# Kernel tuning notes

Measured on AMD Instinct MI355X. Metric: run time of the kernel, lower is better.

Reference implementation:

```python
import jax, jax.numpy as jnp
import numpy as np

N_NODES = 50000
N_EDGES = 800000
IN_C, HID_C, OUT_C, N_CLASSES = 256, 128, 128, 6
N_GRAPHS = 256
BN_EPS = 1e-5


def setup_inputs() -> dict:
    key = jax.random.key(0)
    ks = jax.random.split(key, 24)
    inp = {
        "x": jax.random.normal(ks[0], (N_NODES, IN_C), dtype=jnp.float32),
        "edge_index": jax.random.randint(ks[1], (2, N_EDGES), 0, N_NODES, dtype=jnp.int64),
        "batch": jnp.sort(jax.random.randint(ks[2], (N_NODES,), 0, N_GRAPHS, dtype=jnp.int64)),
    }
    dims = [(IN_C, HID_C), (HID_C, HID_C), (HID_C, OUT_C)]
    k = 3
    for i, (ci, co) in enumerate(dims):
        scale = 1.0 / np.sqrt(ci)
        inp[f"W{i}"] = jax.random.uniform(ks[k], (ci, co), minval=-scale, maxval=scale); k += 1
        inp[f"b{i}"] = jax.random.uniform(ks[k], (co,), minval=-scale, maxval=scale); k += 1
        inp[f"g{i}"] = jax.random.uniform(ks[k], (co,), minval=0.5, maxval=1.5); k += 1
        inp[f"bt{i}"] = 0.1 * jax.random.normal(ks[k], (co,)); k += 1
        inp[f"m{i}"] = 0.1 * jax.random.normal(ks[k], (co,)); k += 1
        inp[f"v{i}"] = jax.random.uniform(ks[k], (co,), minval=0.5, maxval=1.5); k += 1
    scale = 1.0 / np.sqrt(OUT_C)
    inp["lin_W"] = jax.random.uniform(ks[k], (OUT_C, N_CLASSES), minval=-scale, maxval=scale); k += 1
    inp["lin_b"] = jax.random.uniform(ks[k], (N_CLASSES,), minval=-scale, maxval=scale)
    return inp


def gcn_conv(x, W, b, row, col, n):
    # PyG GCNConv: linear transform, add self-loops, symmetric degree norm, scatter-add
    h = x @ W  # [N, Co]
    loop = jnp.arange(n, dtype=row.dtype)
    r = jnp.concatenate([row, loop])
    c = jnp.concatenate([col, loop])
    deg = jax.ops.segment_sum(jnp.ones_like(c, dtype=h.dtype), c, num_segments=n)
    dinv = jax.lax.rsqrt(deg)  # deg >= 1 thanks to self-loops
    norm = dinv[r] * dinv[c]  # [E+N]
    msg = h[r] * norm[:, None]
    return jax.ops.segment_sum(msg, c, num_segments=n) + b


def batch_norm(x, g, bt, m, v):
    return (x - m) * jax.lax.rsqrt(v + BN_EPS) * g + bt


def reference(x, edge_index, batch,
              W0, b0, g0, bt0, m0, v0,
              W1, b1, g1, bt1, m1, v1,
              W2, b2, g2, bt2, m2, v2,
              lin_W, lin_b):
    row, col = edge_index[0], edge_index[1]
    n = x.shape[0]
    params = [(W0, b0, g0, bt0, m0, v0), (W1, b1, g1, bt1, m1, v1), (W2, b2, g2, bt2, m2, v2)]
    h = x
    for (W, b, g, bt, m, v) in params:
        h = gcn_conv(h, W, b, row, col, n)
        h = batch_norm(h, g, bt, m, v)
        h = jax.nn.relu(h)  # dropout is identity in eval mode
    # global mean pool over graphs
    sums = jax.ops.segment_sum(h, batch, num_segments=N_GRAPHS)
    cnts = jax.ops.segment_sum(jnp.ones((n,), dtype=h.dtype), batch, num_segments=N_GRAPHS)
    pooled = sums / jnp.maximum(cnts, 1.0)[:, None]
    return pooled @ lin_W + lin_b  # [N_GRAPHS, N_CLASSES]
```

## Files before the change

kernel.cpp:

```cpp
#include <hip/hip_runtime.h>
#include <hip/hip_bf16.h>

#define N_NODES   50000
#define N_EDGES   800000
#define IN_C      256
#define HID_C     128
#define N_GRAPHS  256
#define N_CLASSES 6
#define BN_EPS    1e-5f

using bf16x8 = __attribute__((ext_vector_type(8))) short;
using f32x4  = __attribute__((ext_vector_type(4))) float;

__device__ __forceinline__ ushort f2bf(float f) {
    union { float f; unsigned u; } v; v.f = f;
    unsigned r = v.u + 0x7fffu + ((v.u >> 16) & 1u);
    return (ushort)(r >> 16);
}
__device__ __forceinline__ float bflo(unsigned u) {
    union { unsigned u; float f; } v; v.u = u << 16; return v.f;
}
__device__ __forceinline__ float bfhi(unsigned u) {
    union { unsigned u; float f; } v; v.u = u & 0xffff0000u; return v.f;
}

__global__ void k_init(int* ecnt, int n) {
    int i = blockIdx.x * blockDim.x + threadIdx.x;
    if (i < n) ecnt[i] = 0;
}

__global__ void k_count_rank(const int* __restrict__ col, int* __restrict__ ecnt,
                             int* __restrict__ rank, int e) {
    int i0 = (blockIdx.x * blockDim.x + threadIdx.x) * 4;
    if (i0 + 3 < e) {
        int4 c = *reinterpret_cast<const int4*>(col + i0);
        int4 r;
        r.x = atomicAdd(&ecnt[c.x], 1);
        r.y = atomicAdd(&ecnt[c.y], 1);
        r.z = atomicAdd(&ecnt[c.z], 1);
        r.w = atomicAdd(&ecnt[c.w], 1);
        *reinterpret_cast<int4*>(rank + i0) = r;
    } else {
        for (int i = i0; i < e; ++i) rank[i] = atomicAdd(&ecnt[col[i]], 1);
    }
}

__global__ void k_scanA(const int* __restrict__ ecnt, int* __restrict__ row_ptr,
                        int* __restrict__ bsum, float* __restrict__ dinv, int n) {
    __shared__ int s[256];
    int t = threadIdx.x;
    int i = blockIdx.x * 256 + t;
    int v = (i < n) ? ecnt[i] : 0;
    if (i < n) dinv[i] = rsqrtf((float)(v + 1));
    s[t] = v;
    __syncthreads();
    for (int d = 1; d < 256; d <<= 1) {
        int add = (t >= d) ? s[t - d] : 0;
        __syncthreads();
        s[t] += add;
        __syncthreads();
    }
    if (i < n) row_ptr[i] = s[t];
    if (t == 255) bsum[blockIdx.x] = s[255];
}

__global__ void k_scanB(const int* __restrict__ bsum, int* __restrict__ bsumx, int nb) {
    __shared__ int s[256];
    int t = threadIdx.x;
    int v = (t < nb) ? bsum[t] : 0;
    s[t] = v;
    __syncthreads();
    for (int d = 1; d < 256; d <<= 1) {
        int add = (t >= d) ? s[t - d] : 0;
        __syncthreads();
        s[t] += add;
        __syncthreads();
    }
    bsumx[t] = s[t] - v;
}

__global__ void k_scanC(const int* __restrict__ ecnt, int* __restrict__ row_ptr,
                        const int* __restrict__ bsumx, int n, int e) {
    int i = blockIdx.x * 256 + threadIdx.x;
    if (i < n) row_ptr[i] = row_ptr[i] - ecnt[i] + bsumx[blockIdx.x];
    if (i == 0) row_ptr[n] = e;
}

__global__ void k_fill(const int* __restrict__ row, const int* __restrict__ col,
                       const int* __restrict__ row_ptr, const int* __restrict__ rank,
                       const float* __restrict__ dinv, int2* __restrict__ wedge, int e) {
    int i0 = (blockIdx.x * blockDim.x + threadIdx.x) * 4;
    if (i0 + 3 < e) {
        int4 c  = *reinterpret_cast<const int4*>(col + i0);
        int4 r  = *reinterpret_cast<const int4*>(row + i0);
        int4 rk = *reinterpret_cast<const int4*>(rank + i0);
        wedge[row_ptr[c.x] + rk.x] = make_int2(r.x, __float_as_int(dinv[r.x]));
        wedge[row_ptr[c.y] + rk.y] = make_int2(r.y, __float_as_int(dinv[r.y]));
        wedge[row_ptr[c.z] + rk.z] = make_int2(r.z, __float_as_int(dinv[r.z]));
        wedge[row_ptr[c.w] + rk.w] = make_int2(r.w, __float_as_int(dinv[r.w]));
    } else {
        for (int i = i0; i < e; ++i)
            wedge[row_ptr[col[i]] + rank[i]] = make_int2(row[i], __float_as_int(dinv[row[i]]));
    }
}

__global__ void k_prepWF(const float* __restrict__ W0, const float* __restrict__ W1,
                         const float* __restrict__ W2, ushort* __restrict__ Wt0,
                         ushort* __restrict__ Wt1, ushort* __restrict__ Wt2,
                         const float* __restrict__ b0, const float* __restrict__ g0,
                         const float* __restrict__ bt0, const float* __restrict__ m0,
                         const float* __restrict__ v0,
                         const float* __restrict__ b1, const float* __restrict__ g1,
                         const float* __restrict__ bt1, const float* __restrict__ m1,
                         const float* __restrict__ v1,
                         const float* __restrict__ b2, const float* __restrict__ g2,
                         const float* __restrict__ bt2, const float* __restrict__ m2,
                         const float* __restrict__ v2,
                         float* __restrict__ fA, float* __restrict__ fC) {
    int t = blockIdx.x * blockDim.x + threadIdx.x;
    const int NW0 = 128 * IN_C, NW1 = 128 * HID_C;
    if (t < NW0) {
        int co = t / IN_C, k = t % IN_C;
        Wt0[t] = f2bf(W0[(size_t)k * 128 + co]);
    } else if (t < NW0 + NW1) {
        int u = t - NW0;
        int co = u / HID_C, k = u % HID_C;
        Wt1[u] = f2bf(W1[(size_t)k * 128 + co]);
    } else if (t < NW0 + 2 * NW1) {
        int u = t - NW0 - NW1;
        int co = u / HID_C, k = u % HID_C;
        Wt2[u] = f2bf(W2[(size_t)k * 128 + co]);
    } else if (t < NW0 + 2 * NW1 + 3 * 128) {
        int u = t - NW0 - 2 * NW1;
        int layer = u >> 7, c = u & 127;
        const float *b_, *g_, *bt_, *m_, *v_;
        if (layer == 0)      { b_ = b0; g_ = g0; bt_ = bt0; m_ = m0; v_ = v0; }
        else if (layer == 1) { b_ = b1; g_ = g1; bt_ = bt1; m_ = m1; v_ = v1; }
        else                 { b_ = b2; g_ = g2; bt_ = bt2; m_ = m2; v_ = v2; }
        float A = g_[c] * rsqrtf(v_[c] + BN_EPS);
        fA[u] = A;
        fC[u] = (b_[c] - m_[c]) * A + bt_[c];
    }
}

template <int K, bool AFP32>
__global__ __launch_bounds__(256) void k_gemmbf(const void* __restrict__ Av,
                                                const ushort* __restrict__ Wt,
                                                ushort* __restrict__ Cbf, int M) {
    extern __shared__ char smem[];
    const int tid = threadIdx.x;
    constexpr int CPC = K / 8;
    constexpr int NCH = 128 * CPC;
    for (int c = tid; c < NCH; c += 256) {
        int col = c / CPC, kg = c % CPC;
        float4 v = *reinterpret_cast<const float4*>(Wt + (size_t)col * K + kg * 8);
        int dst = col * (K * 2) + ((kg * 16) ^ ((col & 7) << 4));
        *reinterpret_cast<float4*>(smem + dst) = v;
    }
    __syncthreads();

    const int wave = tid >> 6, lane = tid & 63;
    const int l15 = lane & 15, lg = lane >> 4;
    const int row = blockIdx.x * 64 + wave * 16 + l15;
    const bool rok = (row < M);

    f32x4 acc[8] = {};

#pragma unroll
    for (int ks = 0; ks < K / 32; ++ks) {
        bf16x8 a;
        if (AFP32) {
            const float* Ap = (const float*)Av + (size_t)row * K + ks * 32 + lg * 8;
            float4 f0, f1;
            if (rok) {
                f0 = *reinterpret_cast<const float4*>(Ap);
                f1 = *reinterpret_cast<const float4*>(Ap + 4);
            } else {
                f0 = make_float4(0, 0, 0, 0); f1 = f0;
            }
            a[0] = (short)f2bf(f0.x); a[1] = (short)f2bf(f0.y);
            a[2] = (short)f2bf(f0.z); a[3] = (short)f2bf(f0.w);
            a[4] = (short)f2bf(f1.x); a[5] = (short)f2bf(f1.y);
            a[6] = (short)f2bf(f1.z); a[7] = (short)f2bf(f1.w);
        } else {
            if (rok) {
                const ushort* Ap = (const ushort*)Av + (size_t)row * K + ks * 32 + lg * 8;
                a = *reinterpret_cast<const bf16x8*>(Ap);
            } else {
#pragma unroll
                for (int j = 0; j < 8; ++j) a[j] = 0;
            }
        }
#pragma unroll
        for (int cf = 0; cf < 8; ++cf) {
            int col = cf * 16 + l15;
            int off = col * (K * 2) + ((ks * 64 + lg * 16) ^ ((col & 7) << 4));
            bf16x8 b = *reinterpret_cast<const bf16x8*>(smem + off);
            acc[cf] = __builtin_amdgcn_mfma_f32_16x16x32_bf16(a, b, acc[cf], 0, 0, 0);
        }
    }

#pragma unroll
    for (int cf = 0; cf < 8; ++cf) {
        int col = cf * 16 + l15;
#pragma unroll
        for (int i = 0; i < 4; ++i) {
            int r = blockIdx.x * 64 + wave * 16 + lg * 4 + i;
            if (r < M) Cbf[(size_t)r * 128 + col] = f2bf(acc[cf][i]);
        }
    }
}

__global__ __launch_bounds__(256) void k_aggbf(const ushort* __restrict__ h,
                                               const int* __restrict__ row_ptr,
                                               const int2* __restrict__ wedge,
                                               const float* __restrict__ dinv,
                                               const float* __restrict__ fA,
                                               const float* __restrict__ fC,
                                               ushort* __restrict__ out, int n) {
    int wave = threadIdx.x >> 6, lane = threadIdx.x & 63;
    int vtx = blockIdx.x * 4 + wave;
    if (vtx >= n) return;
    int q = lane >> 4, l15 = lane & 15;
    int c0 = l15 * 8;
    int beg = row_ptr[vtx], end = row_ptr[vtx + 1];

    float a0 = 0.f, a1 = 0.f, a2 = 0.f, a3 = 0.f;
    float a4 = 0.f, a5 = 0.f, a6 = 0.f, a7 = 0.f;
    for (int e = beg + q; e < end; e += 16) {
        int eB = e + 4, eC = e + 8, eD = e + 12;
        bool kB = eB < end, kC = eC < end, kD = eD < end;
        int2 wd0 = wedge[e];
        int2 wd1 = wedge[kB ? eB : e];
        int2 wd2 = wedge[kC ? eC : e];
        int2 wd3 = wedge[kD ? eD : e];
        float w0 = __int_as_float(wd0.y);
        float w1 = kB ? __int_as_float(wd1.y) : 0.f;
        float w2 = kC ? __int_as_float(wd2.y) : 0.f;
        float w3 = kD ? __int_as_float(wd3.y) : 0.f;
        uint4 u0 = *reinterpret_cast<const uint4*>(h + (size_t)wd0.x * 128 + c0);
        uint4 u1 = *reinterpret_cast<const uint4*>(h + (size_t)wd1.x * 128 + c0);
        uint4 u2 = *reinterpret_cast<const uint4*>(h + (size_t)wd2.x * 128 + c0);
        uint4 u3 = *reinterpret_cast<const uint4*>(h + (size_t)wd3.x * 128 + c0);
        a0 = fmaf(bflo(u0.x), w0, a0); a1 = fmaf(bfhi(u0.x), w0, a1);
        a2 = fmaf(bflo(u0.y), w0, a2); a3 = fmaf(bfhi(u0.y), w0, a3);
        a4 = fmaf(bflo(u0.z), w0, a4); a5 = fmaf(bfhi(u0.z), w0, a5);
        a6 = fmaf(bflo(u0.w), w0, a6); a7 = fmaf(bfhi(u0.w), w0, a7);
        a0 = fmaf(bflo(u1.x), w1, a0); a1 = fmaf(bfhi(u1.x), w1, a1);
        a2 = fmaf(bflo(u1.y), w1, a2); a3 = fmaf(bfhi(u1.y), w1, a3);
        a4 = fmaf(bflo(u1.z), w1, a4); a5 = fmaf(bfhi(u1.z), w1, a5);
        a6 = fmaf(bflo(u1.w), w1, a6); a7 = fmaf(bfhi(u1.w), w1, a7);
        a0 = fmaf(bflo(u2.x), w2, a0); a1 = fmaf(bfhi(u2.x), w2, a1);
        a2 = fmaf(bflo(u2.y), w2, a2); a3 = fmaf(bfhi(u2.y), w2, a3);
        a4 = fmaf(bflo(u2.z), w2, a4); a5 = fmaf(bfhi(u2.z), w2, a5);
        a6 = fmaf(bflo(u2.w), w2, a6); a7 = fmaf(bfhi(u2.w), w2, a7);
        a0 = fmaf(bflo(u3.x), w3, a0); a1 = fmaf(bfhi(u3.x), w3, a1);
        a2 = fmaf(bflo(u3.y), w3, a2); a3 = fmaf(bfhi(u3.y), w3, a3);
        a4 = fmaf(bflo(u3.z), w3, a4); a5 = fmaf(bfhi(u3.z), w3, a5);
        a6 = fmaf(bflo(u3.w), w3, a6); a7 = fmaf(bfhi(u3.w), w3, a7);
    }

    a0 += __shfl_xor(a0, 16); a0 += __shfl_xor(a0, 32);
    a1 += __shfl_xor(a1, 16); a1 += __shfl_xor(a1, 32);
    a2 += __shfl_xor(a2, 16); a2 += __shfl_xor(a2, 32);
    a3 += __shfl_xor(a3, 16); a3 += __shfl_xor(a3, 32);
    a4 += __shfl_xor(a4, 16); a4 += __shfl_xor(a4, 32);
    a5 += __shfl_xor(a5, 16); a5 += __shfl_xor(a5, 32);
    a6 += __shfl_xor(a6, 16); a6 += __shfl_xor(a6, 32);
    a7 += __shfl_xor(a7, 16); a7 += __shfl_xor(a7, 32);

    if (q == 0) {
        float dv = dinv[vtx];
        float dvv = dv * dv;
        uint4 us = *reinterpret_cast<const uint4*>(h + (size_t)vtx * 128 + c0);
        float4 A0 = *reinterpret_cast<const float4*>(fA + c0);
        float4 A1 = *reinterpret_cast<const float4*>(fA + c0 + 4);
        float4 C0 = *reinterpret_cast<const float4*>(fC + c0);
        float4 C1 = *reinterpret_cast<const float4*>(fC + c0 + 4);
        float v0 = fmaf(a0, dv * A0.x, fmaf(bflo(us.x), dvv * A0.x, C0.x));
        float v1 = fmaf(a1, dv * A0.y, fmaf(bfhi(us.x), dvv * A0.y, C0.y));
        float v2 = fmaf(a2, dv * A0.z, fmaf(bflo(us.y), dvv * A0.z, C0.z));
        float v3 = fmaf(a3, dv * A0.w, fmaf(bfhi(us.y), dvv * A0.w, C0.w));
        float v4 = fmaf(a4, dv * A1.x, fmaf(bflo(us.z), dvv * A1.x, C1.x));
        float v5 = fmaf(a5, dv * A1.y, fmaf(bfhi(us.z), dvv * A1.y, C1.y));
        float v6 = fmaf(a6, dv * A1.z, fmaf(bflo(us.w), dvv * A1.z, C1.z));
        float v7 = fmaf(a7, dv * A1.w, fmaf(bfhi(us.w), dvv * A1.w, C1.w));
        v0 = fmaxf(v0, 0.f); v1 = fmaxf(v1, 0.f); v2 = fmaxf(v2, 0.f); v3 = fmaxf(v3, 0.f);
        v4 = fmaxf(v4, 0.f); v5 = fmaxf(v5, 0.f); v6 = fmaxf(v6, 0.f); v7 = fmaxf(v7, 0.f);
        uint4 packed;
        packed.x = (unsigned)f2bf(v0) | ((unsigned)f2bf(v1) << 16);
        packed.y = (unsigned)f2bf(v2) | ((unsigned)f2bf(v3) << 16);
        packed.z = (unsigned)f2bf(v4) | ((unsigned)f2bf(v5) << 16);
        packed.w = (unsigned)f2bf(v6) | ((unsigned)f2bf(v7) << 16);
        *reinterpret_cast<uint4*>(out + (size_t)vtx * 128 + c0) = packed;
    }
}

__global__ __launch_bounds__(256) void k_poolfinal(const ushort* __restrict__ h,
                                                   const int* __restrict__ batch,
                                                   const float* __restrict__ lw,
                                                   const float* __restrict__ lb,
                                                   float* __restrict__ out, int n) {
    __shared__ float psum[4][128];
    __shared__ float pool[128];
    int g = blockIdx.x;
    int tid = threadIdx.x;
    int wave = tid >> 6, lane = tid & 63;
    int lo = 0, hi = n;
    while (lo < hi) { int m = (lo + hi) >> 1; if (batch[m] < g) lo = m + 1; else hi = m; }
    int a = lo;
    lo = 0; hi = n;
    int g1 = g + 1;
    while (lo < hi) { int m = (lo + hi) >> 1; if (batch[m] < g1) lo = m + 1; else hi = m; }
    int b = lo;

    int c0 = lane * 2;
    float a0 = 0.f, a1 = 0.f;
    int i = a + wave;
    for (; i + 12 < b; i += 16) {
        unsigned u0 = *reinterpret_cast<const unsigned*>(h + (size_t)i * 128 + c0);
        unsigned u1 = *reinterpret_cast<const unsigned*>(h + (size_t)(i + 4) * 128 + c0);
        unsigned u2 = *reinterpret_cast<const unsigned*>(h + (size_t)(i + 8) * 128 + c0);
        unsigned u3 = *reinterpret_cast<const unsigned*>(h + (size_t)(i + 12) * 128 + c0);
        a0 += bflo(u0) + bflo(u1) + bflo(u2) + bflo(u3);
        a1 += bfhi(u0) + bfhi(u1) + bfhi(u2) + bfhi(u3);
    }
    for (; i < b; i += 4) {
        unsigned u = *reinterpret_cast<const unsigned*>(h + (size_t)i * 128 + c0);
        a0 += bflo(u); a1 += bfhi(u);
    }
    psum[wave][c0] = a0;
    psum[wave][c0 + 1] = a1;
    __syncthreads();
    if (tid < 128) pool[tid] = psum[0][tid] + psum[1][tid] + psum[2][tid] + psum[3][tid];
    __syncthreads();
    if (tid < N_CLASSES) {
        float inv = 1.0f / fmaxf((float)(b - a), 1.0f);
        float s = 0.f;
        for (int k = 0; k < 128; ++k) s = fmaf(pool[k], lw[k * N_CLASSES + tid], s);
        out[g * N_CLASSES + tid] = s * inv + lb[tid];
    }
}

extern "C" void kernel_launch(void* const* d_in, const int* in_sizes, int n_in,
                              void* d_out, int out_size, void* d_ws, size_t ws_size,
                              hipStream_t stream) {
    const float* x      = (const float*)d_in[0];
    const int*   ei     = (const int*)d_in[1];
    const int*   batch  = (const int*)d_in[2];
    const float* W0  = (const float*)d_in[3];
    const float* b0  = (const float*)d_in[4];
    const float* g0  = (const float*)d_in[5];
    const float* bt0 = (const float*)d_in[6];
    const float* m0  = (const float*)d_in[7];
    const float* v0  = (const float*)d_in[8];
    const float* W1  = (const float*)d_in[9];
    const float* b1  = (const float*)d_in[10];
    const float* g1  = (const float*)d_in[11];
    const float* bt1 = (const float*)d_in[12];
    const float* m1  = (const float*)d_in[13];
    const float* v1  = (const float*)d_in[14];
    const float* W2  = (const float*)d_in[15];
    const float* b2  = (const float*)d_in[16];
    const float* g2  = (const float*)d_in[17];
    const float* bt2 = (const float*)d_in[18];
    const float* m2  = (const float*)d_in[19];
    const float* v2  = (const float*)d_in[20];
    const float* lw  = (const float*)d_in[21];
    const float* lb  = (const float*)d_in[22];
    float* out = (float*)d_out;

    const int N = in_sizes[2];
    const int E = in_sizes[1] / 2;
    const int* row = ei;
    const int* col = ei + E;

    char* ws = (char*)d_ws;
    size_t off = 0;
    auto alloc = [&](size_t bytes) {
        void* p = ws + off;
        off += (bytes + 511) & ~(size_t)511;
        return p;
    };
    ushort* hA     = (ushort*)alloc((size_t)N * 128 * 2);
    ushort* hB     = (ushort*)alloc((size_t)N * 128 * 2);
    ushort* Wt0    = (ushort*)alloc((size_t)128 * IN_C * 2);
    ushort* Wt1    = (ushort*)alloc((size_t)128 * HID_C * 2);
    ushort* Wt2    = (ushort*)alloc((size_t)128 * HID_C * 2);
    int*   ecnt    = (int*)alloc((size_t)N * 4);
    int*   rank    = (int*)alloc((size_t)E * 4);
    int*   row_ptr = (int*)alloc((size_t)(N + 1) * 4);
    int2*  wedge   = (int2*)alloc((size_t)E * 8);
    float* dinv    = (float*)alloc((size_t)N * 4);
    int*   bsum    = (int*)alloc(256 * 4);
    int*   bsumx   = (int*)alloc(256 * 4);
    float* fA      = (float*)alloc(3 * 128 * 4);
    float* fC      = (float*)alloc(3 * 128 * 4);

    const int NB_n  = (N + 255) / 256;
    const int NB_e4 = (E / 4 + 255) / 256;

    k_init<<<NB_n, 256, 0, stream>>>(ecnt, N);
    k_count_rank<<<NB_e4, 256, 0, stream>>>(col, ecnt, rank, E);
    k_scanA<<<NB_n, 256, 0, stream>>>(ecnt, row_ptr, bsum, dinv, N);
    k_scanB<<<1, 256, 0, stream>>>(bsum, bsumx, NB_n);
    k_scanC<<<NB_n, 256, 0, stream>>>(ecnt, row_ptr, bsumx, N, E);
    k_fill<<<NB_e4, 256, 0, stream>>>(row, col, row_ptr, rank, dinv, wedge, E);

    const int PW = (128 * (IN_C + 2 * HID_C) + 3 * 128 + 255) / 256;
    k_prepWF<<<PW, 256, 0, stream>>>(W0, W1, W2, Wt0, Wt1, Wt2,
                                     b0, g0, bt0, m0, v0,
                                     b1, g1, bt1, m1, v1,
                                     b2, g2, bt2, m2, v2, fA, fC);

    const int GB = (N + 63) / 64;
    const int AB = (N + 3) / 4;

    k_gemmbf<IN_C, true><<<GB, 256, IN_C * 128 * 2, stream>>>(x, Wt0, hB, N);
    k_aggbf<<<AB, 256, 0, stream>>>(hB, row_ptr, wedge, dinv, fA, fC, hA, N);
    k_gemmbf<HID_C, false><<<GB, 256, HID_C * 128 * 2, stream>>>(hA, Wt1, hB, N);
    k_aggbf<<<AB, 256, 0, stream>>>(hB, row_ptr, wedge, dinv, fA + 128, fC + 128, hA, N);
    k_gemmbf<HID_C, false><<<GB, 256, HID_C * 128 * 2, stream>>>(hA, Wt2, hB, N);
    k_aggbf<<<AB, 256, 0, stream>>>(hB, row_ptr, wedge, dinv, fA + 256, fC + 256, hA, N);

    k_poolfinal<<<N_GRAPHS, 256, 0, stream>>>(hA, batch, lw, lb, out, N);
}
```

Baseline: 228.1 us.

## Slice hidden features into 32-column planes for cache-local aggregation; merge setup kernels

Stores intermediate bf16 features as four column slices of 32 channels each, [4][N][32]. The aggregation kernel now processes one slice per block, with 16 lanes covering one vertex's 32 channels, so each gathered row is 64 bytes and a slice's working set is a quarter of the full feature matrix, which should improve L2 hit rates on the random neighbour gathers. The GEMM's A reads and C writes and the pooling reads are changed to match the sliced layout. Separately, the ecnt zeroing is folded into the weight-prep kernel and the two scan-fixup kernels are merged, removing two launches. In exchange, each vertex's edge list is now walked four times, once per slice, and the wedge indices are reloaded for each pass.

```diff
diff --git a/kernel.cpp b/kernel.cpp
--- a/kernel.cpp
+++ b/kernel.cpp
@@ -9,6 +9,7 @@
 #define N_CLASSES 6
 #define BN_EPS    1e-5f
 
+
 using bf16x8 = __attribute__((ext_vector_type(8))) short;
 using f32x4  = __attribute__((ext_vector_type(4))) float;
 
@@ -22,11 +23,6 @@
 }
 __device__ __forceinline__ float bfhi(unsigned u) {
     union { unsigned u; float f; } v; v.u = u & 0xffff0000u; return v.f;
-}
-
-__global__ void k_init(int* ecnt, int n) {
-    int i = blockIdx.x * blockDim.x + threadIdx.x;
-    if (i < n) ecnt[i] = 0;
 }
 
 __global__ void k_count_rank(const int* __restrict__ col, int* __restrict__ ecnt,
@@ -64,7 +60,8 @@
     if (t == 255) bsum[blockIdx.x] = s[255];
 }
 
-__global__ void k_scanB(const int* __restrict__ bsum, int* __restrict__ bsumx, int nb) {
+__global__ void k_scanC(const int* __restrict__ ecnt, int* __restrict__ row_ptr,
+                        const int* __restrict__ bsum, int nb, int n, int e) {
     __shared__ int s[256];
     int t = threadIdx.x;
     int v = (t < nb) ? bsum[t] : 0;
@@ -76,13 +73,9 @@
         s[t] += add;
         __syncthreads();
     }
-    bsumx[t] = s[t] - v;
-}
-
-__global__ void k_scanC(const int* __restrict__ ecnt, int* __restrict__ row_ptr,
-                        const int* __restrict__ bsumx, int n, int e) {
-    int i = blockIdx.x * 256 + threadIdx.x;
-    if (i < n) row_ptr[i] = row_ptr[i] - ecnt[i] + bsumx[blockIdx.x];
+    int off = (blockIdx.x > 0) ? s[blockIdx.x - 1] : 0;
+    int i = blockIdx.x * 256 + t;
+    if (i < n) row_ptr[i] = row_ptr[i] - ecnt[i] + off;
     if (i == 0) row_ptr[n] = e;
 }
 
@@ -116,8 +109,10 @@
                          const float* __restrict__ b2, const float* __restrict__ g2,
                          const float* __restrict__ bt2, const float* __restrict__ m2,
                          const float* __restrict__ v2,
-                         float* __restrict__ fA, float* __restrict__ fC) {
+                         float* __restrict__ fA, float* __restrict__ fC,
+                         int* __restrict__ ecnt, int n) {
     int t = blockIdx.x * blockDim.x + threadIdx.x;
+    if (t < n) ecnt[t] = 0;
     const int NW0 = 128 * IN_C, NW1 = 128 * HID_C;
     if (t < NW0) {
         int co = t / IN_C, k = t % IN_C;
@@ -184,7 +179,7 @@
             a[6] = (short)f2bf(f1.z); a[7] = (short)f2bf(f1.w);
         } else {
             if (rok) {
-                const ushort* Ap = (const ushort*)Av + (size_t)row * K + ks * 32 + lg * 8;
+                const ushort* Ap = (const ushort*)Av + (size_t)ks * M * 32 + (size_t)row * 32 + lg * 8;
                 a = *reinterpret_cast<const bf16x8*>(Ap);
             } else {
 #pragma unroll
@@ -202,11 +197,12 @@
 
 #pragma unroll
     for (int cf = 0; cf < 8; ++cf) {
-        int col = cf * 16 + l15;
+        int sl = cf >> 1;
+        int off = (cf & 1) * 16 + l15;
 #pragma unroll
         for (int i = 0; i < 4; ++i) {
             int r = blockIdx.x * 64 + wave * 16 + lg * 4 + i;
-            if (r < M) Cbf[(size_t)r * 128 + col] = f2bf(acc[cf][i]);
+            if (r < M) Cbf[(size_t)sl * M * 32 + (size_t)r * 32 + off] = f2bf(acc[cf][i]);
         }
     }
 }
@@ -218,82 +214,49 @@
                                                const float* __restrict__ fA,
                                                const float* __restrict__ fC,
                                                ushort* __restrict__ out, int n) {
-    int wave = threadIdx.x >> 6, lane = threadIdx.x & 63;
-    int vtx = blockIdx.x * 4 + wave;
+    const int slice = blockIdx.x & 3;
+    const int nb = blockIdx.x >> 2;
+    const int wave = threadIdx.x >> 6, lane = threadIdx.x & 63;
+    const int q = lane >> 4, l15 = lane & 15;
+    const int vtx = nb * 16 + wave * 4 + q;
     if (vtx >= n) return;
-    int q = lane >> 4, l15 = lane & 15;
-    int c0 = l15 * 8;
+    const ushort* hs = h + (size_t)slice * n * 32;
+    const int c0 = l15 * 2;
+
     int beg = row_ptr[vtx], end = row_ptr[vtx + 1];
-
-    float a0 = 0.f, a1 = 0.f, a2 = 0.f, a3 = 0.f;
-    float a4 = 0.f, a5 = 0.f, a6 = 0.f, a7 = 0.f;
-    for (int e = beg + q; e < end; e += 16) {
-        int eB = e + 4, eC = e + 8, eD = e + 12;
-        bool kB = eB < end, kC = eC < end, kD = eD < end;
+    float a0 = 0.f, a1 = 0.f;
+    for (int e = beg; e < end; e += 4) {
+        int e1 = e + 1, e2 = e + 2, e3 = e + 3;
+        bool k1 = e1 < end, k2 = e2 < end, k3 = e3 < end;
         int2 wd0 = wedge[e];
-        int2 wd1 = wedge[kB ? eB : e];
-        int2 wd2 = wedge[kC ? eC : e];
-        int2 wd3 = wedge[kD ? eD : e];
+        int2 wd1 = wedge[k1 ? e1 : e];
+        int2 wd2 = wedge[k2 ? e2 : e];
+        int2 wd3 = wedge[k3 ? e3 : e];
         float w0 = __int_as_float(wd0.y);
-        float w1 = kB ? __int_as_float(wd1.y) : 0.f;
-        float w2 = kC ? __int_as_float(wd2.y) : 0.f;
-        float w3 = kD ? __int_as_float(wd3.y) : 0.f;
-        uint4 u0 = *reinterpret_cast<const uint4*>(h + (size_t)wd0.x * 128 + c0);
-        uint4 u1 = *reinterpret_cast<const uint4*>(h + (size_t)wd1.x * 128 + c0);
-        uint4 u2 = *reinterpret_cast<const uint4*>(h + (size_t)wd2.x * 128 + c0);
-        uint4 u3 = *reinterpret_cast<const uint4*>(h + (size_t)wd3.x * 128 + c0);
-        a0 = fmaf(bflo(u0.x), w0, a0); a1 = fmaf(bfhi(u0.x), w0, a1);
-        a2 = fmaf(bflo(u0.y), w0, a2); a3 = fmaf(bfhi(u0.y), w0, a3);
-        a4 = fmaf(bflo(u0.z), w0, a4); a5 = fmaf(bfhi(u0.z), w0, a5);
-        a6 = fmaf(bflo(u0.w), w0, a6); a7 = fmaf(bfhi(u0.w), w0, a7);
-        a0 = fmaf(bflo(u1.x), w1, a0); a1 = fmaf(bfhi(u1.x), w1, a1);
-        a2 = fmaf(bflo(u1.y), w1, a2); a3 = fmaf(bfhi(u1.y), w1, a3);
-        a4 = fmaf(bflo(u1.z), w1, a4); a5 = fmaf(bfhi(u1.z), w1, a5);
-        a6 = fmaf(bflo(u1.w), w1, a6); a7 = fmaf(bfhi(u1.w), w1, a7);
-        a0 = fmaf(bflo(u2.x), w2, a0); a1 = fmaf(bfhi(u2.x), w2, a1);
-        a2 = fmaf(bflo(u2.y), w2, a2); a3 = fmaf(bfhi(u2.y), w2, a3);
-        a4 = fmaf(bflo(u2.z), w2, a4); a5 = fmaf(bfhi(u2.z), w2, a5);
-        a6 = fmaf(bflo(u2.w), w2, a6); a7 = fmaf(bfhi(u2.w), w2, a7);
-        a0 = fmaf(bflo(u3.x), w3, a0); a1 = fmaf(bfhi(u3.x), w3, a1);
-        a2 = fmaf(bflo(u3.y), w3, a2); a3 = fmaf(bfhi(u3.y), w3, a3);
-        a4 = fmaf(bflo(u3.z), w3, a4); a5 = fmaf(bfhi(u3.z), w3, a5);
-        a6 = fmaf(bflo(u3.w), w3, a6); a7 = fmaf(bfhi(u3.w), w3, a7);
-    }
-
-    a0 += __shfl_xor(a0, 16); a0 += __shfl_xor(a0, 32);
-    a1 += __shfl_xor(a1, 16); a1 += __shfl_xor(a1, 32);
-    a2 += __shfl_xor(a2, 16); a2 += __shfl_xor(a2, 32);
-    a3 += __shfl_xor(a3, 16); a3 += __shfl_xor(a3, 32);
-    a4 += __shfl_xor(a4, 16); a4 += __shfl_xor(a4, 32);
-    a5 += __shfl_xor(a5, 16); a5 += __shfl_xor(a5, 32);
-    a6 += __shfl_xor(a6, 16); a6 += __shfl_xor(a6, 32);
-    a7 += __shfl_xor(a7, 16); a7 += __shfl_xor(a7, 32);
-
-    if (q == 0) {
-        float dv = dinv[vtx];
-        float dvv = dv * dv;
-        uint4 us = *reinterpret_cast<const uint4*>(h + (size_t)vtx * 128 + c0);
-        float4 A0 = *reinterpret_cast<const float4*>(fA + c0);
-        float4 A1 = *reinterpret_cast<const float4*>(fA + c0 + 4);
-        float4 C0 = *reinterpret_cast<const float4*>(fC + c0);
-        float4 C1 = *reinterpret_cast<const float4*>(fC + c0 + 4);
-        float v0 = fmaf(a0, dv * A0.x, fmaf(bflo(us.x), dvv * A0.x, C0.x));
-        float v1 = fmaf(a1, dv * A0.y, fmaf(bfhi(us.x), dvv * A0.y, C0.y));
-        float v2 = fmaf(a2, dv * A0.z, fmaf(bflo(us.y), dvv * A0.z, C0.z));
-        float v3 = fmaf(a3, dv * A0.w, fmaf(bfhi(us.y), dvv * A0.w, C0.w));
-        float v4 = fmaf(a4, dv * A1.x, fmaf(bflo(us.z), dvv * A1.x, C1.x));
-        float v5 = fmaf(a5, dv * A1.y, fmaf(bfhi(us.z), dvv * A1.y, C1.y));
-        float v6 = fmaf(a6, dv * A1.z, fmaf(bflo(us.w), dvv * A1.z, C1.z));
-        float v7 = fmaf(a7, dv * A1.w, fmaf(bfhi(us.w), dvv * A1.w, C1.w));
-        v0 = fmaxf(v0, 0.f); v1 = fmaxf(v1, 0.f); v2 = fmaxf(v2, 0.f); v3 = fmaxf(v3, 0.f);
-        v4 = fmaxf(v4, 0.f); v5 = fmaxf(v5, 0.f); v6 = fmaxf(v6, 0.f); v7 = fmaxf(v7, 0.f);
-        uint4 packed;
-        packed.x = (unsigned)f2bf(v0) | ((unsigned)f2bf(v1) << 16);
-        packed.y = (unsigned)f2bf(v2) | ((unsigned)f2bf(v3) << 16);
-        packed.z = (unsigned)f2bf(v4) | ((unsigned)f2bf(v5) << 16);
-        packed.w = (unsigned)f2bf(v6) | ((unsigned)f2bf(v7) << 16);
-        *reinterpret_cast<uint4*>(out + (size_t)vtx * 128 + c0) = packed;
-    }
+        float w1 = k1 ? __int_as_float(wd1.y) : 0.f;
+        float w2 = k2 ? __int_as_float(wd2.y) : 0.f;
+        float w3 = k3 ? __int_as_float(wd3.y) : 0.f;
+        unsigned u0 = *reinterpret_cast<const unsigned*>(hs + (size_t)wd0.x * 32 + c0);
+        unsigned u1 = *reinterpret_cast<const unsigned*>(hs + (size_t)wd1.x * 32 + c0);
+        unsigned u2 = *reinterpret_cast<const unsigned*>(hs + (size_t)wd2.x * 32 + c0);
+        unsigned u3 = *reinterpret_cast<const unsigned*>(hs + (size_t)wd3.x * 32 + c0);
+        a0 = fmaf(bflo(u0), w0, a0); a1 = fmaf(bfhi(u0), w0, a1);
+        a0 = fmaf(bflo(u1), w1, a0); a1 = fmaf(bfhi(u1), w1, a1);
+        a0 = fmaf(bflo(u2), w2, a0); a1 = fmaf(bfhi(u2), w2, a1);
+        a0 = fmaf(bflo(u3), w3, a0); a1 = fmaf(bfhi(u3), w3, a1);
+    }
+
+    float dv = dinv[vtx];
+    float dvv = dv * dv;
+    unsigned us = *reinterpret_cast<const unsigned*>(hs + (size_t)vtx * 32 + c0);
+    int c = slice * 32 + c0;
+    float2 A = *reinterpret_cast<const float2*>(fA + c);
+    float2 C = *reinterpret_cast<const float2*>(fC + c);
+    float v0 = fmaf(a0, dv * A.x, fmaf(bflo(us), dvv * A.x, C.x));
+    float v1 = fmaf(a1, dv * A.y, fmaf(bfhi(us), dvv * A.y, C.y));
+    v0 = fmaxf(v0, 0.f); v1 = fmaxf(v1, 0.f);
+    unsigned packed = (unsigned)f2bf(v0) | ((unsigned)f2bf(v1) << 16);
+    *reinterpret_cast<unsigned*>(out + (size_t)slice * n * 32 + (size_t)vtx * 32 + c0) = packed;
 }
 
 __global__ __launch_bounds__(256) void k_poolfinal(const ushort* __restrict__ h,
@@ -314,21 +277,22 @@
     while (lo < hi) { int m = (lo + hi) >> 1; if (batch[m] < g1) lo = m + 1; else hi = m; }
     int b = lo;
 
-    int c0 = lane * 2;
+    const ushort* hs = h + (size_t)(lane >> 4) * n * 32 + (lane & 15) * 2;
     float a0 = 0.f, a1 = 0.f;
     int i = a + wave;
     for (; i + 12 < b; i += 16) {
-        unsigned u0 = *reinterpret_cast<const unsigned*>(h + (size_t)i * 128 + c0);
-        unsigned u1 = *reinterpret_cast<const unsigned*>(h + (size_t)(i + 4) * 128 + c0);
-        unsigned u2 = *reinterpret_cast<const unsigned*>(h + (size_t)(i + 8) * 128 + c0);
-        unsigned u3 = *reinterpret_cast<const unsigned*>(h + (size_t)(i + 12) * 128 + c0);
+        unsigned u0 = *reinterpret_cast<const unsigned*>(hs + (size_t)i * 32);
+        unsigned u1 = *reinterpret_cast<const unsigned*>(hs + (size_t)(i + 4) * 32);
+        unsigned u2 = *reinterpret_cast<const unsigned*>(hs + (size_t)(i + 8) * 32);
+        unsigned u3 = *reinterpret_cast<const unsigned*>(hs + (size_t)(i + 12) * 32);
         a0 += bflo(u0) + bflo(u1) + bflo(u2) + bflo(u3);
         a1 += bfhi(u0) + bfhi(u1) + bfhi(u2) + bfhi(u3);
     }
     for (; i < b; i += 4) {
-        unsigned u = *reinterpret_cast<const unsigned*>(h + (size_t)i * 128 + c0);
+        unsigned u = *reinterpret_cast<const unsigned*>(hs + (size_t)i * 32);
         a0 += bflo(u); a1 += bfhi(u);
     }
+    int c0 = lane * 2;
     psum[wave][c0] = a0;
     psum[wave][c0 + 1] = a1;
     __syncthreads();
@@ -393,28 +357,24 @@
     int2*  wedge   = (int2*)alloc((size_t)E * 8);
     float* dinv    = (float*)alloc((size_t)N * 4);
     int*   bsum    = (int*)alloc(256 * 4);
-    int*   bsumx   = (int*)alloc(256 * 4);
     float* fA      = (float*)alloc(3 * 128 * 4);
     float* fC      = (float*)alloc(3 * 128 * 4);
 
     const int NB_n  = (N + 255) / 256;
     const int NB_e4 = (E / 4 + 255) / 256;
-
-    k_init<<<NB_n, 256, 0, stream>>>(ecnt, N);
-    k_count_rank<<<NB_e4, 256, 0, stream>>>(col, ecnt, rank, E);
-    k_scanA<<<NB_n, 256, 0, stream>>>(ecnt, row_ptr, bsum, dinv, N);
-    k_scanB<<<1, 256, 0, stream>>>(bsum, bsumx, NB_n);
-    k_scanC<<<NB_n, 256, 0, stream>>>(ecnt, row_ptr, bsumx, N, E);
-    k_fill<<<NB_e4, 256, 0, stream>>>(row, col, row_ptr, rank, dinv, wedge, E);
 
     const int PW = (128 * (IN_C + 2 * HID_C) + 3 * 128 + 255) / 256;
     k_prepWF<<<PW, 256, 0, stream>>>(W0, W1, W2, Wt0, Wt1, Wt2,
                                      b0, g0, bt0, m0, v0,
                                      b1, g1, bt1, m1, v1,
-                                     b2, g2, bt2, m2, v2, fA, fC);
+                                     b2, g2, bt2, m2, v2, fA, fC, ecnt, N);
+    k_count_rank<<<NB_e4, 256, 0, stream>>>(col, ecnt, rank, E);
+    k_scanA<<<NB_n, 256, 0, stream>>>(ecnt, row_ptr, bsum, dinv, N);
+    k_scanC<<<NB_n, 256, 0, stream>>>(ecnt, row_ptr, bsum, NB_n, N, E);
+    k_fill<<<NB_e4, 256, 0, stream>>>(row, col, row_ptr, rank, dinv, wedge, E);
 
     const int GB = (N + 63) / 64;
-    const int AB = (N + 3) / 4;
+    const int AB = 4 * ((N + 15) / 16);
 
     k_gemmbf<IN_C, true><<<GB, 256, IN_C * 128 * 2, stream>>>(x, Wt0, hB, N);
     k_aggbf<<<AB, 256, 0, stream>>>(hB, row_ptr, wedge, dinv, fA, fC, hA, N);
```

Measured after the change: 281.9 us. 1.24x slower.
